# Performance work log

Hardware: AMD Instinct MI355X
Metric: run time of the kernel (lower is better)

The kernel has to match this reference:

```python
import jax, jax.numpy as jnp
import numpy as np

ALPHA = 0.1       # args.alpha
T = 1.0           # args.T temperature
SIGMA = 64.0      # Gaussian kernel bandwidth of kernel_function
B_CONST = 1.0     # B in get_lambda
N_ITERS = 50      # 2^-50 << tol=1e-8, matches the break condition of the 1000-iter loop
HW = 256          # image resolution (upsample target)


def _features(feat):
    # get_feature: bilinear upsample (align_corners=False == half-pixel, as jax.image.resize) then sigmoid(x/T)
    n, c, _, _ = feat.shape
    up = jax.image.resize(feat, (n, c, HW, HW), method='bilinear')
    return jax.nn.sigmoid(up / T)


def setup_inputs() -> dict:
    key = jax.random.key(0)
    k1, k2, k3, k4 = jax.random.split(key, 4)
    return {
        'cal_feat': jax.random.normal(k1, (256, 1, 64, 64), jnp.float32),
        'test_feat': jax.random.normal(k2, (32, 1, 64, 64), jnp.float32),
        'cal_gt': jax.random.randint(k3, (256, 1, 256, 256), 0, 2, jnp.int32),
        'test_gt': jax.random.randint(k4, (32, 1, 256, 256), 0, 2, jnp.int32),
    }


def reference(cal_feat, test_feat, cal_gt, test_gt):
    cal_res = _features(cal_feat)    # [N,1,H,W] in (0,1)
    test_res = _features(test_feat)  # [B,1,H,W]
    N = cal_res.shape[0]
    B = test_res.shape[0]
    f32 = cal_res.dtype

    # kernel_function.get_weight: Gaussian RBF on flattened features, plus self-weight 1, row-normalized -> [B, N+1]
    cf = cal_res.reshape(N, -1)
    tf = test_res.reshape(B, -1)
    d2 = (tf * tf).sum(-1)[:, None] + (cf * cf).sum(-1)[None, :] - 2.0 * (tf @ cf.T)
    k = jnp.exp(-d2 / (2.0 * SIGMA * SIGMA))
    w = jnp.concatenate([k, jnp.ones((B, 1), f32)], axis=1)
    w = w / w.sum(axis=1, keepdims=True)

    # FNR_i(t) = #{positive pixels of cal sample i with score < t} / #positives
    # (pred = res >= t, so false negatives are positive pixels with res < t). Precompute sorted
    # positive-pixel scores per cal sample so the bisection is a batched searchsorted.
    gt = (cal_gt > 0).reshape(N, -1)
    pos = jnp.sum(gt, axis=1)                                    # [N]
    scores = jnp.where(gt, cal_res.reshape(N, -1), jnp.inf)
    sorted_scores = jnp.sort(scores, axis=1)                     # [N, HW*HW], padding at +inf
    pos_f = jnp.maximum(pos, 1).astype(f32)

    def fnr_at(t):  # t: [B] thresholds -> [N, B]
        cnt = jax.vmap(lambda s: jnp.searchsorted(s, t, side='left'))(sorted_scores)
        return cnt.astype(f32) / pos_f[:, None]

    # batched bisection on lambda (get_lambda, vectorized over the B test samples)
    def body(carry, _):
        low, high = carry
        lam = 0.5 * (low + high)
        fnr = fnr_at(1.0 - lam)                                   # [N, B]
        risk = jnp.einsum('bn,nb->b', w[:, :-1], fnr) + w[:, -1] * B_CONST
        high = jnp.where(risk < ALPHA, lam, high)
        low = jnp.where(risk >= ALPHA, lam, low)
        return (low, high), None

    init = (jnp.zeros((B,), f32), jnp.ones((B,), f32))
    (low, _), _ = jax.lax.scan(body, init, None, length=N_ITERS)
    lam = low  # _lambda = low after the loop

    # prediction set, size and per-test FNR (get_fnr_list on the test sample)
    pred = test_res >= (1.0 - lam)[:, None, None, None]           # [B,1,H,W] bool
    size = jnp.sum(pred, axis=(1, 2, 3)).astype(f32)
    tgt = test_gt > 0
    tp = jnp.sum(pred & tgt, axis=(1, 2, 3)).astype(f32)
    tpos = jnp.maximum(jnp.sum(tgt, axis=(1, 2, 3)), 1).astype(f32)
    fnr_test = 1.0 - tp / tpos                                    # fdr_tensor, [B]
    return fnr_test, lam, size
```

## Files before the change

kernel.cpp:

```cpp
#include <hip/hip_runtime.h>


#define NPIX 65536
#define HB 16256
#define CDF_STRIDE 16272
#define ALPHA 0.1f
#define STAGE_CAP 40960

#define OFF_TESTRES  0
#define OFF_CALBF    8388608u
#define OFF_TESTBF   41943040u
#define OFF_GROUPED  46137344u
#define OFF_CDF      79691776u
#define OFF_GPART    96354304u
#define OFF_CC       98451456u
#define OFF_TT       98452480u
#define OFF_THR      98452608u
#define OFF_LAM      98452736u
#define OFF_FACC     98452864u

typedef __attribute__((ext_vector_type(8))) short bf16x8;
typedef __attribute__((ext_vector_type(16))) float f32x16;

__device__ __forceinline__ unsigned short f2bf_rne(float f) {
  unsigned u = __float_as_uint(f);
  return (unsigned short)((u + 0x7FFFu + ((u >> 16) & 1u)) >> 16);
}

__device__ __forceinline__ int SW(int w) { return w ^ ((w >> 5) & 31); }

__device__ __forceinline__ float score_at(const float* __restrict__ sfeat,
                                          int x0, int x1, float wx, int y) {
  float sy = 0.25f * (float)y - 0.375f;
  int y0 = (int)floorf(sy);
  float wy = sy - (float)y0;
  int y1 = y0 + 1;
  if (y0 < 0) y0 = 0;
  if (y1 > 63) y1 = 63;
  float a = sfeat[y0 * 64 + x0] * (1.f - wx) + sfeat[y0 * 64 + x1] * wx;
  float b = sfeat[y1 * 64 + x0] * (1.f - wx) + sfeat[y1 * 64 + x1] * wx;
  float v = a * (1.f - wy) + b * wy;
  return 1.f / (1.f + __expf(-v));
}

__global__ __launch_bounds__(1024, 2) void k_calt(const float* __restrict__ featc,
                                                  const int* __restrict__ gt,
                                                  unsigned short* __restrict__ calbf,
                                                  unsigned* __restrict__ cdf,
                                                  unsigned short* __restrict__ grouped,
                                                  float* __restrict__ cc,
                                                  const float* __restrict__ featt,
                                                  float* __restrict__ tres,
                                                  unsigned short* __restrict__ tbf) {
  __shared__ unsigned smem[9264];
  __shared__ float sfeat[4096];
  __shared__ float tfeat[4096];
  __shared__ unsigned short sstage[STAGE_CAP];
  const int tid = threadIdx.x;
  const int lane = tid & 63, wv = tid >> 6;
  const int x = tid & 255, yq = tid >> 8;
  float sx = 0.25f * (float)x - 0.375f;
  int x0 = (int)floorf(sx);
  float wx = sx - (float)x0;
  int x1 = x0 + 1;
  if (x0 < 0) x0 = 0;
  if (x1 > 63) x1 = 63;

  const int n = blockIdx.x;
  const int b = n >> 3, sl = n & 7;
  for (int i = tid; i < 8192; i += 1024) smem[i] = 0;
  for (int i = tid; i < 4096; i += 1024) {
    sfeat[i] = featc[n * 4096 + i];
    tfeat[i] = featt[b * 4096 + i];
  }
  const int* gtn = gt + (size_t)n * NPIX;
  unsigned short* cbn = calbf + (size_t)n * NPIX;
  __syncthreads();

  {
    float* resb = tres + (size_t)b * NPIX + sl * 8192;
    unsigned short* tbn = tbf + (size_t)b * NPIX + sl * 8192;
    #pragma unroll
    for (int i = 0; i < 8; ++i) {
      int y = sl * 32 + i * 4 + yq;
      float s = score_at(tfeat, x0, x1, wx, y);
      int q = i * 1024 + tid;
      resb[q] = s;
      tbn[q] = f2bf_rne(s);
    }
  }

  unsigned long long pm = 0ull;
  float sumsq = 0.f;
  #pragma unroll 8
  for (int it = 0; it < 64; ++it) {
    int y = it * 4 + yq;
    float s = score_at(sfeat, x0, x1, wx, y);
    int p = (y << 8) + x;
    unsigned short bh = f2bf_rne(s);
    cbn[p] = bh;
    float sr = __uint_as_float((unsigned)bh << 16);
    sumsq += sr * sr;
    if (gtn[p] > 0) {
      pm |= (1ull << it);
      unsigned bits = __float_as_uint(s);
      atomicAdd(&smem[SW((int)(bits >> 17))], (bits & 0x10000u) ? 0x10000u : 1u);
    }
  }
  #pragma unroll
  for (int off = 32; off; off >>= 1) sumsq += __shfl_xor(sumsq, off);
  if (lane == 0) smem[8208 + wv] = __float_as_uint(sumsq);
  __syncthreads();
  if (tid == 0) {
    float c = 0.f;
    for (int w = 0; w < 16; ++w) c += __uint_as_float(smem[8208 + w]);
    cc[n] = c;
  }
  const int wbase = tid * 8;
  unsigned psum = 0;
  #pragma unroll
  for (int j = 0; j < 8; ++j) {
    unsigned w = smem[SW(wbase + j)];
    psum += (w & 0xFFFFu) + (w >> 16);
  }
  unsigned inc = psum;
  #pragma unroll
  for (int off = 1; off < 64; off <<= 1) {
    unsigned v = __shfl_up(inc, off);
    if (lane >= off) inc += v;
  }
  if (lane == 63) smem[8192 + wv] = inc;
  smem[8224 + tid] = inc - psum;
  __syncthreads();
  {
    unsigned woff = 0;
    for (int w = 0; w < wv; ++w) woff += smem[8192 + w];
    unsigned run = woff + smem[8224 + tid];
    #pragma unroll
    for (int j = 0; j < 8; ++j) {
      int si = SW(wbase + j);
      unsigned w = smem[si];
      unsigned clo = run;
      run += (w & 0xFFFFu);
      unsigned chi = run;
      run += (w >> 16);
      smem[si] = (chi << 16) | clo;
    }
    if (tid == 1023) smem[9248] = run;
  }
  __syncthreads();
  unsigned* cdfn = cdf + (size_t)n * CDF_STRIDE;
  for (int i = tid; i < HB; i += 1024) {
    unsigned w = smem[SW(i >> 1)];
    cdfn[i] = (i & 1) ? (w >> 16) : (w & 0xFFFFu);
  }
  const unsigned pos = smem[9248];
  if (tid == 0) cdfn[HB] = pos;
  __syncthreads();
  unsigned short* gn = grouped + (size_t)n * NPIX;
  for (int it = 0; it < 64; ++it) {
    if (pm & (1ull << it)) {
      int y = it * 4 + yq;
      float s = score_at(sfeat, x0, x1, wx, y);
      unsigned bits = __float_as_uint(s);
      unsigned old = atomicAdd(&smem[SW((int)(bits >> 17))], (bits & 0x10000u) ? 0x10000u : 1u);
      unsigned idx = (bits & 0x10000u) ? (old >> 16) : (old & 0xFFFFu);
      unsigned short lo = (unsigned short)(bits & 0xFFFFu);
      if (idx < STAGE_CAP) sstage[idx] = lo;
      else gn[idx] = lo;
    }
  }
  __syncthreads();
  unsigned lim = pos < STAGE_CAP ? pos : STAGE_CAP;
  for (unsigned i = tid; i < lim; i += 1024) gn[i] = sstage[i];
}

__global__ __launch_bounds__(1024) void k_tt(const unsigned short* __restrict__ tbf,
                                             float* __restrict__ tt) {
  __shared__ unsigned smem[16];
  const int tid = threadIdx.x;
  const int lane = tid & 63, wv = tid >> 6;
  const int x = tid & 255, yq = tid >> 8;
  const int b = blockIdx.x;
  const unsigned short* tbn = tbf + (size_t)b * NPIX;
  float sumsq = 0.f;
  #pragma unroll 4
  for (int it = 0; it < 64; ++it) {
    int p = ((it * 4 + yq) << 8) + x;
    float sr = __uint_as_float((unsigned)tbn[p] << 16);
    sumsq += sr * sr;
  }
  #pragma unroll
  for (int off = 32; off; off >>= 1) sumsq += __shfl_xor(sumsq, off);
  if (lane == 0) smem[wv] = __float_as_uint(sumsq);
  __syncthreads();
  if (tid == 0) {
    float t = 0.f;
    for (int w = 0; w < 16; ++w) t += __uint_as_float(smem[w]);
    tt[b] = t;
  }
}

__global__ __launch_bounds__(256) void k_gemm(const unsigned short* __restrict__ tbf,
                                              const unsigned short* __restrict__ cbf,
                                              float* __restrict__ gpart) {
  __shared__ __align__(16) unsigned short As[16384];
  __shared__ __align__(16) unsigned short Bs[16384];
  __shared__ float lred[4][1024];
  const int tid = threadIdx.x;
  const int lane = tid & 63, wv = tid >> 6;
  const int r = lane & 31, half = lane >> 5;
  const int nt = blockIdx.x;
  f32x16 acc;
  #pragma unroll
  for (int i = 0; i < 16; ++i) acc[i] = 0.f;
  for (int ch = 0; ch < 2; ++ch) {
    const size_t kbase = (size_t)blockIdx.y * 1024 + ch * 512;
    __syncthreads();
    #pragma unroll
    for (int s = 0; s < 16; ++s) {
      int flat = s * 256 + tid;
      int rem = flat & 2047;
      int row = rem >> 6, kb = rem & 63;
      const unsigned short* src = (flat >= 2048)
          ? cbf + (size_t)(nt * 32 + row) * NPIX + kbase + kb * 8
          : tbf + (size_t)row * NPIX + kbase + kb * 8;
      int slot = ((kb << 5) + row) ^ (kb & 31);
      int4 v = *(const int4*)src;
      *(int4*)((flat >= 2048 ? Bs : As) + slot * 8) = v;
    }
    __syncthreads();
    #pragma unroll
    for (int i = 0; i < 8; ++i) {
      int k8 = (wv << 4) + i * 2 + half;
      int slot = ((k8 << 5) + r) ^ (k8 & 31);
      bf16x8 a = *(const bf16x8*)(As + slot * 8);
      bf16x8 b = *(const bf16x8*)(Bs + slot * 8);
      acc = __builtin_amdgcn_mfma_f32_32x32x16_bf16(a, b, acc, 0, 0, 0);
    }
  }
  #pragma unroll
  for (int rg = 0; rg < 16; ++rg) {
    int m = (rg & 3) + 8 * (rg >> 2) + 4 * half;
    lred[wv][m * 32 + r] = acc[rg];
  }
  __syncthreads();
  float* gp = gpart + (size_t)(blockIdx.y * 8 + nt) * 1024;
  for (int e = tid; e < 1024; e += 256)
    gp[e] = lred[0][e] + lred[1][e] + lred[2][e] + lred[3][e];
}

__global__ __launch_bounds__(512) void k_quant(const float* __restrict__ gpart,
                                               const float* __restrict__ cc,
                                               const float* __restrict__ tt,
                                               const unsigned* __restrict__ cdf,
                                               const unsigned short* __restrict__ grouped,
                                               float* __restrict__ lam,
                                               float* __restrict__ thr,
                                               int* __restrict__ facc) {
  __shared__ float qs[256];
  __shared__ float bins[4096];
  __shared__ float red[8];
  __shared__ float bc[2];
  __shared__ unsigned sBin;
  const int b = blockIdx.x, tid = threadIdx.x;
  const int lane = tid & 63, wv = tid >> 6;

  if (tid < 4) facc[b * 4 + tid] = 0;
  for (int i = tid; i < 4096; i += 512) bins[i] = 0.f;
  if (tid == 0) sBin = 0xFFFFFFFFu;

  float k = 0.f;
  if (tid < 256) {
    const float* gp = gpart + ((tid >> 5) * 1024) + (b * 32) + (tid & 31);
    float g = 0.f;
    #pragma unroll 8
    for (int ks = 0; ks < 64; ++ks) g += gp[(size_t)ks * 8192];
    float d2 = tt[b] + cc[tid] - 2.f * g;
    k = expf(-d2 * (1.f / 8192.f));
  }
  float v = k;
  #pragma unroll
  for (int off = 32; off; off >>= 1) v += __shfl_xor(v, off);
  if (lane == 0) red[wv] = v;
  __syncthreads();
  if (tid == 0) {
    float ws = 1.f;
    for (int w = 0; w < 8; ++w) ws += red[w];
    bc[0] = ws;
  }
  __syncthreads();
  const float wsum = bc[0];
  const float wlast = 1.f / wsum;
  const float R = ALPHA - wlast;
  if (R <= 0.f) {
    if (tid == 0) { lam[b] = 1.0f; thr[b] = 0.0f; }
    return;
  }
  if (tid < 256) {
    unsigned pos = cdf[(size_t)tid * CDF_STRIDE + HB];
    qs[tid] = k / (wsum * (float)(pos ? pos : 1u));
  }
  __syncthreads();

  int lo = 0, hi = HB;
  float baseS = 0.f;
  for (int it = 0; it < 14; ++it) {
    int mid = (lo + hi) >> 1;
    float p = 0.f;
    if (tid < 256) p = qs[tid] * (float)cdf[(size_t)tid * CDF_STRIDE + mid];
    float r = p;
    #pragma unroll
    for (int off = 32; off; off >>= 1) r += __shfl_xor(r, off);
    if (lane == 0) red[wv] = r;
    __syncthreads();
    if (tid == 0) {
      float s = 0.f;
      for (int w = 0; w < 8; ++w) s += red[w];
      bc[1] = s;
    }
    __syncthreads();
    float S = bc[1];
    if (S < R) { lo = mid; baseS = S; } else { hi = mid; }
  }
  const int B = lo;

  {
    const int n = tid >> 1;
    const float q = qs[n];
    const unsigned* cn = cdf + (size_t)n * CDF_STRIDE;
    const unsigned short* gn = grouped + (size_t)n * NPIX;
    unsigned e0 = cn[B + 1];
    for (unsigned j = cn[B] + (tid & 1); j < e0; j += 2)
      atomicAdd(&bins[gn[j] >> 4], q);
  }
  __syncthreads();

  if (wv == 0) {
    float s = 0.f;
    for (int j = 0; j < 64; ++j) s += bins[lane * 64 + j];
    float inc = s;
    #pragma unroll
    for (int off = 1; off < 64; off <<= 1) {
      float u = __shfl_up(inc, off);
      if (lane >= off) inc += u;
    }
    float pre = inc - s;
    bool hit = (baseS + pre < R) && (baseS + inc >= R);
    unsigned long long m = __ballot(hit);
    int ow = m ? (__ffsll((unsigned long long)m) - 1) : -1;
    if (lane == ow) {
      float run = baseS + pre;
      unsigned bin = (unsigned)lane * 64 + 63;
      for (int j = 0; j < 64; ++j) {
        float bv = bins[lane * 64 + j];
        if (run + bv >= R) { bin = (unsigned)lane * 64 + j; break; }
        run += bv;
      }
      sBin = bin;
    }
    if (m == 0 && lane == 0) sBin = 4095u;
  }
  __syncthreads();
  if (tid == 0) {
    unsigned tb = ((unsigned)B << 16) | (sBin << 4);
    lam[b] = 1.0f - __uint_as_float(tb | 0x8u);
    thr[b] = __uint_as_float((tb | 0xFu) + 1u);
  }
}

__global__ __launch_bounds__(256) void k_finalp(const float* __restrict__ tres,
                                                const int* __restrict__ tgt,
                                                const float* __restrict__ thr,
                                                int* __restrict__ facc) {
  __shared__ int red[12];
  const int b = blockIdx.x, seg = blockIdx.y, tid = threadIdx.x;
  const int lane = tid & 63, wv = tid >> 6;
  const float th = thr[b];
  const float4* rb4 = (const float4*)(tres + (size_t)b * NPIX + seg * 8192);
  const int4* gb4 = (const int4*)(tgt + (size_t)b * NPIX + seg * 8192);
  int sz = 0, tp = 0, tpos = 0;
  #pragma unroll
  for (int i = 0; i < 8; ++i) {
    float4 r4 = rb4[i * 256 + tid];
    int4 g4 = gb4[i * 256 + tid];
    int p0 = (r4.x >= th), t0 = (g4.x > 0);
    int p1 = (r4.y >= th), t1 = (g4.y > 0);
    int p2 = (r4.z >= th), t2 = (g4.z > 0);
    int p3 = (r4.w >= th), t3 = (g4.w > 0);
    sz += p0 + p1 + p2 + p3;
    tp += (p0 & t0) + (p1 & t1) + (p2 & t2) + (p3 & t3);
    tpos += t0 + t1 + t2 + t3;
  }
  #pragma unroll
  for (int off = 32; off; off >>= 1) {
    sz += __shfl_xor(sz, off);
    tp += __shfl_xor(tp, off);
    tpos += __shfl_xor(tpos, off);
  }
  if (lane == 0) { red[wv] = sz; red[4 + wv] = tp; red[8 + wv] = tpos; }
  __syncthreads();
  if (tid == 0) {
    int s0 = red[0] + red[1] + red[2] + red[3];
    int s1 = red[4] + red[5] + red[6] + red[7];
    int s2 = red[8] + red[9] + red[10] + red[11];
    atomicAdd(&facc[b * 4 + 0], s0);
    atomicAdd(&facc[b * 4 + 1], s1);
    atomicAdd(&facc[b * 4 + 2], s2);
  }
}

__global__ void k_out(const int* __restrict__ facc, const float* __restrict__ lam,
                      float* __restrict__ out) {
  int b = threadIdx.x;
  if (b < 32) {
    int sz = facc[b * 4], tp = facc[b * 4 + 1], tpos = facc[b * 4 + 2];
    float tposf = (float)(tpos > 0 ? tpos : 1);
    out[b] = 1.f - (float)tp / tposf;
    out[32 + b] = lam[b];
    out[64 + b] = (float)sz;
  }
}

extern "C" void kernel_launch(void* const* d_in, const int* in_sizes, int n_in,
                              void* d_out, int out_size, void* d_ws, size_t ws_size,
                              hipStream_t stream) {
  const float* cal_feat = (const float*)d_in[0];
  const float* test_feat = (const float*)d_in[1];
  const int* cal_gt = (const int*)d_in[2];
  const int* test_gt = (const int*)d_in[3];
  float* out = (float*)d_out;
  char* ws = (char*)d_ws;

  float* test_res = (float*)(ws + OFF_TESTRES);
  unsigned short* cal_bf = (unsigned short*)(ws + OFF_CALBF);
  unsigned short* test_bf = (unsigned short*)(ws + OFF_TESTBF);
  unsigned short* grouped = (unsigned short*)(ws + OFF_GROUPED);
  unsigned* cdf = (unsigned*)(ws + OFF_CDF);
  float* gpart = (float*)(ws + OFF_GPART);
  float* cc = (float*)(ws + OFF_CC);
  float* tt = (float*)(ws + OFF_TT);
  float* thr = (float*)(ws + OFF_THR);
  float* lam = (float*)(ws + OFF_LAM);
  int* facc = (int*)(ws + OFF_FACC);

  k_calt<<<dim3(256), dim3(1024), 0, stream>>>(cal_feat, cal_gt, cal_bf, cdf, grouped, cc,
                                               test_feat, test_res, test_bf);
  k_tt<<<dim3(32), dim3(1024), 0, stream>>>(test_bf, tt);
  k_gemm<<<dim3(8, 64), dim3(256), 0, stream>>>(test_bf, cal_bf, gpart);
  k_quant<<<dim3(32), dim3(512), 0, stream>>>(gpart, cc, tt, cdf, grouped, lam, thr, facc);
  k_finalp<<<dim3(32, 8), dim3(256), 0, stream>>>(test_res, test_gt, thr, facc);
  k_out<<<dim3(1), dim3(64), 0, stream>>>(facc, lam, out);
}
```

Baseline: 246.9 us.

## Fuse test norm, quantile search, final stats and output into one kernel

Folds the test squared-norm reduction, threshold search, per-test FNR/size accumulation and output writing into a single kernel, removing three launches and the global atomics and intermediate buffers between them. Separately, the upsample in k_calt now reuses each horizontally interpolated row across consecutive output rows in a rolling fashion instead of recomputing both source rows per pixel. The final pass now runs over 32 blocks instead of 256, so the 8 MB test score/gt scan gets less parallelism and may take longer than the separate kernel did.

```diff
diff --git a/kernel.cpp b/kernel.cpp
--- a/kernel.cpp
+++ b/kernel.cpp
@@ -14,10 +14,6 @@
 #define OFF_CDF      79691776u
 #define OFF_GPART    96354304u
 #define OFF_CC       98451456u
-#define OFF_TT       98452480u
-#define OFF_THR      98452608u
-#define OFF_LAM      98452736u
-#define OFF_FACC     98452864u
 
 typedef __attribute__((ext_vector_type(8))) short bf16x8;
 typedef __attribute__((ext_vector_type(16))) float f32x16;
@@ -29,6 +25,14 @@
 
 __device__ __forceinline__ int SW(int w) { return w ^ ((w >> 5) & 31); }
 
+__device__ __forceinline__ float hrow_at(const float* __restrict__ f, int x0, int x1,
+                                         float wx, int r) {
+  return f[r * 64 + x0] * (1.f - wx) + f[r * 64 + x1] * wx;
+}
+__device__ __forceinline__ float sig_v(float a, float b, float wy) {
+  float v = a * (1.f - wy) + b * wy;
+  return 1.f / (1.f + __expf(-v));
+}
 __device__ __forceinline__ float score_at(const float* __restrict__ sfeat,
                                           int x0, int x1, float wx, int y) {
   float sy = 0.25f * (float)y - 0.375f;
@@ -37,10 +41,9 @@
   int y1 = y0 + 1;
   if (y0 < 0) y0 = 0;
   if (y1 > 63) y1 = 63;
-  float a = sfeat[y0 * 64 + x0] * (1.f - wx) + sfeat[y0 * 64 + x1] * wx;
-  float b = sfeat[y1 * 64 + x0] * (1.f - wx) + sfeat[y1 * 64 + x1] * wx;
-  float v = a * (1.f - wy) + b * wy;
-  return 1.f / (1.f + __expf(-v));
+  float a = hrow_at(sfeat, x0, x1, wx, y0);
+  float b = hrow_at(sfeat, x0, x1, wx, y1);
+  return sig_v(a, b, wy);
 }
 
 __global__ __launch_bounds__(1024, 2) void k_calt(const float* __restrict__ featc,
@@ -65,6 +68,9 @@
   int x1 = x0 + 1;
   if (x0 < 0) x0 = 0;
   if (x1 > 63) x1 = 63;
+  const float syq = 0.25f * (float)yq - 0.375f;
+  const int c0 = (int)floorf(syq);
+  const float wy = syq - (float)c0;
 
   const int n = blockIdx.x;
   const int b = n >> 3, sl = n & 7;
@@ -80,10 +86,16 @@
   {
     float* resb = tres + (size_t)b * NPIX + sl * 8192;
     unsigned short* tbn = tbf + (size_t)b * NPIX + sl * 8192;
+    int r0 = sl * 8 + c0;
+    if (r0 < 0) r0 = 0;
+    float hprev = hrow_at(tfeat, x0, x1, wx, r0);
     #pragma unroll
     for (int i = 0; i < 8; ++i) {
-      int y = sl * 32 + i * 4 + yq;
-      float s = score_at(tfeat, x0, x1, wx, y);
+      int r1 = sl * 8 + i + c0 + 1;
+      if (r1 > 63) r1 = 63;
+      float hb = hrow_at(tfeat, x0, x1, wx, r1);
+      float s = sig_v(hprev, hb, wy);
+      hprev = hb;
       int q = i * 1024 + tid;
       resb[q] = s;
       tbn[q] = f2bf_rne(s);
@@ -92,19 +104,26 @@
 
   unsigned long long pm = 0ull;
   float sumsq = 0.f;
-  #pragma unroll 8
-  for (int it = 0; it < 64; ++it) {
-    int y = it * 4 + yq;
-    float s = score_at(sfeat, x0, x1, wx, y);
-    int p = (y << 8) + x;
-    unsigned short bh = f2bf_rne(s);
-    cbn[p] = bh;
-    float sr = __uint_as_float((unsigned)bh << 16);
-    sumsq += sr * sr;
-    if (gtn[p] > 0) {
-      pm |= (1ull << it);
-      unsigned bits = __float_as_uint(s);
-      atomicAdd(&smem[SW((int)(bits >> 17))], (bits & 0x10000u) ? 0x10000u : 1u);
+  {
+    int r0 = c0 < 0 ? 0 : c0;
+    float hprev = hrow_at(sfeat, x0, x1, wx, r0);
+    #pragma unroll 8
+    for (int it = 0; it < 64; ++it) {
+      int r1 = it + c0 + 1;
+      if (r1 > 63) r1 = 63;
+      float hb = hrow_at(sfeat, x0, x1, wx, r1);
+      float s = sig_v(hprev, hb, wy);
+      hprev = hb;
+      int p = ((it * 4 + yq) << 8) + x;
+      unsigned short bh = f2bf_rne(s);
+      cbn[p] = bh;
+      float sr = __uint_as_float((unsigned)bh << 16);
+      sumsq += sr * sr;
+      if (gtn[p] > 0) {
+        pm |= (1ull << it);
+        unsigned bits = __float_as_uint(s);
+        atomicAdd(&smem[SW((int)(bits >> 17))], (bits & 0x10000u) ? 0x10000u : 1u);
+      }
     }
   }
   #pragma unroll
@@ -173,32 +192,6 @@
   __syncthreads();
   unsigned lim = pos < STAGE_CAP ? pos : STAGE_CAP;
   for (unsigned i = tid; i < lim; i += 1024) gn[i] = sstage[i];
-}
-
-__global__ __launch_bounds__(1024) void k_tt(const unsigned short* __restrict__ tbf,
-                                             float* __restrict__ tt) {
-  __shared__ unsigned smem[16];
-  const int tid = threadIdx.x;
-  const int lane = tid & 63, wv = tid >> 6;
-  const int x = tid & 255, yq = tid >> 8;
-  const int b = blockIdx.x;
-  const unsigned short* tbn = tbf + (size_t)b * NPIX;
-  float sumsq = 0.f;
-  #pragma unroll 4
-  for (int it = 0; it < 64; ++it) {
-    int p = ((it * 4 + yq) << 8) + x;
-    float sr = __uint_as_float((unsigned)tbn[p] << 16);
-    sumsq += sr * sr;
-  }
-  #pragma unroll
-  for (int off = 32; off; off >>= 1) sumsq += __shfl_xor(sumsq, off);
-  if (lane == 0) smem[wv] = __float_as_uint(sumsq);
-  __syncthreads();
-  if (tid == 0) {
-    float t = 0.f;
-    for (int w = 0; w < 16; ++w) t += __uint_as_float(smem[w]);
-    tt[b] = t;
-  }
 }
 
 __global__ __launch_bounds__(256) void k_gemm(const unsigned short* __restrict__ tbf,
@@ -250,33 +243,62 @@
     gp[e] = lred[0][e] + lred[1][e] + lred[2][e] + lred[3][e];
 }
 
-__global__ __launch_bounds__(512) void k_quant(const float* __restrict__ gpart,
-                                               const float* __restrict__ cc,
-                                               const float* __restrict__ tt,
-                                               const unsigned* __restrict__ cdf,
-                                               const unsigned short* __restrict__ grouped,
-                                               float* __restrict__ lam,
-                                               float* __restrict__ thr,
-                                               int* __restrict__ facc) {
+__global__ __launch_bounds__(512) void k_quantf(const float* __restrict__ gpart,
+                                                const float* __restrict__ cc,
+                                                const unsigned short* __restrict__ tbf,
+                                                const unsigned* __restrict__ cdf,
+                                                const unsigned short* __restrict__ grouped,
+                                                const float* __restrict__ tres,
+                                                const int* __restrict__ tgt,
+                                                float* __restrict__ out) {
   __shared__ float qs[256];
   __shared__ float bins[4096];
   __shared__ float red[8];
-  __shared__ float bc[2];
+  __shared__ float tpart[16];
+  __shared__ float bc[6];
+  __shared__ int ired[24];
   __shared__ unsigned sBin;
   const int b = blockIdx.x, tid = threadIdx.x;
   const int lane = tid & 63, wv = tid >> 6;
 
-  if (tid < 4) facc[b * 4 + tid] = 0;
   for (int i = tid; i < 4096; i += 512) bins[i] = 0.f;
   if (tid == 0) sBin = 0xFFFFFFFFu;
 
+  {
+    const unsigned short* tbn = tbf + (size_t)b * NPIX;
+    const int xa = tid & 255, ya = tid >> 8;
+    const int yb = ya + 2;
+    float sa = 0.f, sb = 0.f;
+    #pragma unroll 4
+    for (int it = 0; it < 64; ++it) {
+      float ra = __uint_as_float((unsigned)tbn[((it * 4 + ya) << 8) + xa] << 16);
+      float rb = __uint_as_float((unsigned)tbn[((it * 4 + yb) << 8) + xa] << 16);
+      sa += ra * ra;
+      sb += rb * rb;
+    }
+    #pragma unroll
+    for (int off = 32; off; off >>= 1) {
+      sa += __shfl_xor(sa, off);
+      sb += __shfl_xor(sb, off);
+    }
+    if (lane == 0) { tpart[wv] = sa; tpart[8 + wv] = sb; }
+  }
+  __syncthreads();
+  if (tid == 0) {
+    float t = 0.f;
+    for (int w = 0; w < 16; ++w) t += tpart[w];
+    bc[2] = t;
+  }
+  float g = 0.f;
+  if (tid < 256) {
+    const float* gp = gpart + ((tid >> 5) * 1024) + (b * 32) + (tid & 31);
+    #pragma unroll 8
+    for (int ks = 0; ks < 64; ++ks) g += gp[(size_t)ks * 8192];
+  }
+  __syncthreads();
   float k = 0.f;
   if (tid < 256) {
-    const float* gp = gpart + ((tid >> 5) * 1024) + (b * 32) + (tid & 31);
-    float g = 0.f;
-    #pragma unroll 8
-    for (int ks = 0; ks < 64; ++ks) g += gp[(size_t)ks * 8192];
-    float d2 = tt[b] + cc[tid] - 2.f * g;
+    float d2 = bc[2] + cc[tid] - 2.f * g;
     k = expf(-d2 * (1.f / 8192.f));
   }
   float v = k;
@@ -293,97 +315,89 @@
   const float wsum = bc[0];
   const float wlast = 1.f / wsum;
   const float R = ALPHA - wlast;
-  if (R <= 0.f) {
-    if (tid == 0) { lam[b] = 1.0f; thr[b] = 0.0f; }
-    return;
-  }
-  if (tid < 256) {
-    unsigned pos = cdf[(size_t)tid * CDF_STRIDE + HB];
-    qs[tid] = k / (wsum * (float)(pos ? pos : 1u));
-  }
-  __syncthreads();
-
-  int lo = 0, hi = HB;
-  float baseS = 0.f;
-  for (int it = 0; it < 14; ++it) {
-    int mid = (lo + hi) >> 1;
-    float p = 0.f;
-    if (tid < 256) p = qs[tid] * (float)cdf[(size_t)tid * CDF_STRIDE + mid];
-    float r = p;
-    #pragma unroll
-    for (int off = 32; off; off >>= 1) r += __shfl_xor(r, off);
-    if (lane == 0) red[wv] = r;
+
+  if (R > 0.f) {
+    if (tid < 256) {
+      unsigned pos = cdf[(size_t)tid * CDF_STRIDE + HB];
+      qs[tid] = k / (wsum * (float)(pos ? pos : 1u));
+    }
+    __syncthreads();
+    int lo = 0, hi = HB;
+    float baseS = 0.f;
+    for (int it = 0; it < 14; ++it) {
+      int mid = (lo + hi) >> 1;
+      float p = 0.f;
+      if (tid < 256) p = qs[tid] * (float)cdf[(size_t)tid * CDF_STRIDE + mid];
+      float r = p;
+      #pragma unroll
+      for (int off = 32; off; off >>= 1) r += __shfl_xor(r, off);
+      if (lane == 0) red[wv] = r;
+      __syncthreads();
+      if (tid == 0) {
+        float s = 0.f;
+        for (int w = 0; w < 8; ++w) s += red[w];
+        bc[1] = s;
+      }
+      __syncthreads();
+      float S = bc[1];
+      if (S < R) { lo = mid; baseS = S; } else { hi = mid; }
+    }
+    const int B = lo;
+
+    {
+      const int n = tid >> 1;
+      const float q = qs[n];
+      const unsigned* cn = cdf + (size_t)n * CDF_STRIDE;
+      const unsigned short* gn = grouped + (size_t)n * NPIX;
+      unsigned e0 = cn[B + 1];
+      for (unsigned j = cn[B] + (tid & 1); j < e0; j += 2)
+        atomicAdd(&bins[gn[j] >> 4], q);
+    }
+    __syncthreads();
+
+    if (wv == 0) {
+      float s = 0.f;
+      for (int j = 0; j < 64; ++j) s += bins[lane * 64 + j];
+      float inc = s;
+      #pragma unroll
+      for (int off = 1; off < 64; off <<= 1) {
+        float u = __shfl_up(inc, off);
+        if (lane >= off) inc += u;
+      }
+      float pre = inc - s;
+      bool hit = (baseS + pre < R) && (baseS + inc >= R);
+      unsigned long long m = __ballot(hit);
+      int ow = m ? (__ffsll((unsigned long long)m) - 1) : -1;
+      if (lane == ow) {
+        float run = baseS + pre;
+        unsigned bin = (unsigned)lane * 64 + 63;
+        for (int j = 0; j < 64; ++j) {
+          float bv = bins[lane * 64 + j];
+          if (run + bv >= R) { bin = (unsigned)lane * 64 + j; break; }
+          run += bv;
+        }
+        sBin = bin;
+      }
+      if (m == 0 && lane == 0) sBin = 4095u;
+    }
     __syncthreads();
     if (tid == 0) {
-      float s = 0.f;
-      for (int w = 0; w < 8; ++w) s += red[w];
-      bc[1] = s;
-    }
-    __syncthreads();
-    float S = bc[1];
-    if (S < R) { lo = mid; baseS = S; } else { hi = mid; }
-  }
-  const int B = lo;
-
-  {
-    const int n = tid >> 1;
-    const float q = qs[n];
-    const unsigned* cn = cdf + (size_t)n * CDF_STRIDE;
-    const unsigned short* gn = grouped + (size_t)n * NPIX;
-    unsigned e0 = cn[B + 1];
-    for (unsigned j = cn[B] + (tid & 1); j < e0; j += 2)
-      atomicAdd(&bins[gn[j] >> 4], q);
-  }
-  __syncthreads();
-
-  if (wv == 0) {
-    float s = 0.f;
-    for (int j = 0; j < 64; ++j) s += bins[lane * 64 + j];
-    float inc = s;
-    #pragma unroll
-    for (int off = 1; off < 64; off <<= 1) {
-      float u = __shfl_up(inc, off);
-      if (lane >= off) inc += u;
-    }
-    float pre = inc - s;
-    bool hit = (baseS + pre < R) && (baseS + inc >= R);
-    unsigned long long m = __ballot(hit);
-    int ow = m ? (__ffsll((unsigned long long)m) - 1) : -1;
-    if (lane == ow) {
-      float run = baseS + pre;
-      unsigned bin = (unsigned)lane * 64 + 63;
-      for (int j = 0; j < 64; ++j) {
-        float bv = bins[lane * 64 + j];
-        if (run + bv >= R) { bin = (unsigned)lane * 64 + j; break; }
-        run += bv;
-      }
-      sBin = bin;
-    }
-    if (m == 0 && lane == 0) sBin = 4095u;
-  }
-  __syncthreads();
-  if (tid == 0) {
-    unsigned tb = ((unsigned)B << 16) | (sBin << 4);
-    lam[b] = 1.0f - __uint_as_float(tb | 0x8u);
-    thr[b] = __uint_as_float((tb | 0xFu) + 1u);
-  }
-}
-
-__global__ __launch_bounds__(256) void k_finalp(const float* __restrict__ tres,
-                                                const int* __restrict__ tgt,
-                                                const float* __restrict__ thr,
-                                                int* __restrict__ facc) {
-  __shared__ int red[12];
-  const int b = blockIdx.x, seg = blockIdx.y, tid = threadIdx.x;
-  const int lane = tid & 63, wv = tid >> 6;
-  const float th = thr[b];
-  const float4* rb4 = (const float4*)(tres + (size_t)b * NPIX + seg * 8192);
-  const int4* gb4 = (const int4*)(tgt + (size_t)b * NPIX + seg * 8192);
+      unsigned tb = ((unsigned)B << 16) | (sBin << 4);
+      bc[5] = 1.0f - __uint_as_float(tb | 0x8u);
+      bc[3] = __uint_as_float((tb | 0xFu) + 1u);
+    }
+  } else {
+    if (tid == 0) { bc[5] = 1.0f; bc[3] = 0.0f; }
+  }
+  __syncthreads();
+
+  const float th = bc[3];
+  const float4* rb4 = (const float4*)(tres + (size_t)b * NPIX);
+  const int4* gb4 = (const int4*)(tgt + (size_t)b * NPIX);
   int sz = 0, tp = 0, tpos = 0;
-  #pragma unroll
-  for (int i = 0; i < 8; ++i) {
-    float4 r4 = rb4[i * 256 + tid];
-    int4 g4 = gb4[i * 256 + tid];
+  for (int i = tid; i < 16384; i += 512) {
+    float4 r4 = rb4[i];
+    int4 g4 = gb4[i];
     int p0 = (r4.x >= th), t0 = (g4.x > 0);
     int p1 = (r4.y >= th), t1 = (g4.y > 0);
     int p2 = (r4.z >= th), t2 = (g4.z > 0);
@@ -398,27 +412,15 @@
     tp += __shfl_xor(tp, off);
     tpos += __shfl_xor(tpos, off);
   }
-  if (lane == 0) { red[wv] = sz; red[4 + wv] = tp; red[8 + wv] = tpos; }
+  if (lane == 0) { ired[wv] = sz; ired[8 + wv] = tp; ired[16 + wv] = tpos; }
   __syncthreads();
   if (tid == 0) {
-    int s0 = red[0] + red[1] + red[2] + red[3];
-    int s1 = red[4] + red[5] + red[6] + red[7];
-    int s2 = red[8] + red[9] + red[10] + red[11];
-    atomicAdd(&facc[b * 4 + 0], s0);
-    atomicAdd(&facc[b * 4 + 1], s1);
-    atomicAdd(&facc[b * 4 + 2], s2);
-  }
-}
-
-__global__ void k_out(const int* __restrict__ facc, const float* __restrict__ lam,
-                      float* __restrict__ out) {
-  int b = threadIdx.x;
-  if (b < 32) {
-    int sz = facc[b * 4], tp = facc[b * 4 + 1], tpos = facc[b * 4 + 2];
-    float tposf = (float)(tpos > 0 ? tpos : 1);
-    out[b] = 1.f - (float)tp / tposf;
-    out[32 + b] = lam[b];
-    out[64 + b] = (float)sz;
+    int s0 = 0, s1 = 0, s2 = 0;
+    for (int w = 0; w < 8; ++w) { s0 += ired[w]; s1 += ired[8 + w]; s2 += ired[16 + w]; }
+    float tposf = (float)(s2 > 0 ? s2 : 1);
+    out[b] = 1.f - (float)s1 / tposf;
+    out[32 + b] = bc[5];
+    out[64 + b] = (float)s0;
   }
 }
 
@@ -439,16 +441,10 @@
   unsigned* cdf = (unsigned*)(ws + OFF_CDF);
   float* gpart = (float*)(ws + OFF_GPART);
   float* cc = (float*)(ws + OFF_CC);
-  float* tt = (float*)(ws + OFF_TT);
-  float* thr = (float*)(ws + OFF_THR);
-  float* lam = (float*)(ws + OFF_LAM);
-  int* facc = (int*)(ws + OFF_FACC);
 
   k_calt<<<dim3(256), dim3(1024), 0, stream>>>(cal_feat, cal_gt, cal_bf, cdf, grouped, cc,
                                                test_feat, test_res, test_bf);
-  k_tt<<<dim3(32), dim3(1024), 0, stream>>>(test_bf, tt);
   k_gemm<<<dim3(8, 64), dim3(256), 0, stream>>>(test_bf, cal_bf, gpart);
-  k_quant<<<dim3(32), dim3(512), 0, stream>>>(gpart, cc, tt, cdf, grouped, lam, thr, facc);
-  k_finalp<<<dim3(32, 8), dim3(256), 0, stream>>>(test_res, test_gt, thr, facc);
-  k_out<<<dim3(1), dim3(64), 0, stream>>>(facc, lam, out);
-}
+  k_quantf<<<dim3(32), dim3(512), 0, stream>>>(gpart, cc, test_bf, cdf, grouped,
+                                               test_res, test_gt, out);
+}
```

Result: slower. 254.2 us (+3.0%).

## Fold test sum-of-squares into quantile kernel and widen histogram counters to 32 bits

Applied to the files above, without the earlier changes.

Removes the separate k_tt launch: the test-row squared-norm reduction now runs inside the quantile kernel (renamed k_quantw) on 512 threads, and its loads of gpart are overlapped with that reduction. In the calibration kernel the 16-bit packed histogram counters become full 32-bit bins. This removes the pack/unpack logic in both the scan and the scatter passes. The extra shared memory is paid for by aliasing the test-feature buffer onto the staging buffer and shrinking the staging capacity, so more of the scatter may fall back to global writes. The goal is to cut one launch and some ALU work in the scan/scatter.

```diff
diff --git a/kernel.cpp b/kernel.cpp
--- a/kernel.cpp
+++ b/kernel.cpp
@@ -5,7 +5,7 @@
 #define HB 16256
 #define CDF_STRIDE 16272
 #define ALPHA 0.1f
-#define STAGE_CAP 40960
+#define STAGE_CAP 35840
 
 #define OFF_TESTRES  0
 #define OFF_CALBF    8388608u
@@ -14,10 +14,9 @@
 #define OFF_CDF      79691776u
 #define OFF_GPART    96354304u
 #define OFF_CC       98451456u
-#define OFF_TT       98452480u
-#define OFF_THR      98452608u
-#define OFF_LAM      98452736u
-#define OFF_FACC     98452864u
+#define OFF_THR      98452480u
+#define OFF_LAM      98452608u
+#define OFF_FACC     98452736u
 
 typedef __attribute__((ext_vector_type(8))) short bf16x8;
 typedef __attribute__((ext_vector_type(16))) float f32x16;
@@ -52,10 +51,10 @@
                                                   const float* __restrict__ featt,
                                                   float* __restrict__ tres,
                                                   unsigned short* __restrict__ tbf) {
-  __shared__ unsigned smem[9264];
+  __shared__ unsigned smem[17313];
   __shared__ float sfeat[4096];
-  __shared__ float tfeat[4096];
-  __shared__ unsigned short sstage[STAGE_CAP];
+  __shared__ __align__(16) unsigned short sstage[STAGE_CAP];
+  float* tfeat = (float*)sstage;
   const int tid = threadIdx.x;
   const int lane = tid & 63, wv = tid >> 6;
   const int x = tid & 255, yq = tid >> 8;
@@ -68,7 +67,7 @@
 
   const int n = blockIdx.x;
   const int b = n >> 3, sl = n & 7;
-  for (int i = tid; i < 8192; i += 1024) smem[i] = 0;
+  for (int i = tid; i < HB; i += 1024) smem[i] = 0;
   for (int i = tid; i < 4096; i += 1024) {
     sfeat[i] = featc[n * 4096 + i];
     tfeat[i] = featt[b * 4096 + i];
@@ -103,25 +102,23 @@
     sumsq += sr * sr;
     if (gtn[p] > 0) {
       pm |= (1ull << it);
-      unsigned bits = __float_as_uint(s);
-      atomicAdd(&smem[SW((int)(bits >> 17))], (bits & 0x10000u) ? 0x10000u : 1u);
+      atomicAdd(&smem[SW((int)(__float_as_uint(s) >> 16))], 1u);
     }
   }
   #pragma unroll
   for (int off = 32; off; off >>= 1) sumsq += __shfl_xor(sumsq, off);
-  if (lane == 0) smem[8208 + wv] = __float_as_uint(sumsq);
+  if (lane == 0) smem[16272 + wv] = __float_as_uint(sumsq);
   __syncthreads();
   if (tid == 0) {
     float c = 0.f;
-    for (int w = 0; w < 16; ++w) c += __uint_as_float(smem[8208 + w]);
+    for (int w = 0; w < 16; ++w) c += __uint_as_float(smem[16272 + w]);
     cc[n] = c;
   }
-  const int wbase = tid * 8;
+  const int base = tid * 16;
   unsigned psum = 0;
-  #pragma unroll
-  for (int j = 0; j < 8; ++j) {
-    unsigned w = smem[SW(wbase + j)];
-    psum += (w & 0xFFFFu) + (w >> 16);
+  if (tid < 1016) {
+    #pragma unroll
+    for (int j = 0; j < 16; ++j) psum += smem[SW(base + j)];
   }
   unsigned inc = psum;
   #pragma unroll
@@ -129,32 +126,28 @@
     unsigned v = __shfl_up(inc, off);
     if (lane >= off) inc += v;
   }
-  if (lane == 63) smem[8192 + wv] = inc;
-  smem[8224 + tid] = inc - psum;
+  if (lane == 63) smem[16256 + wv] = inc;
+  smem[16288 + tid] = inc - psum;
   __syncthreads();
   {
     unsigned woff = 0;
-    for (int w = 0; w < wv; ++w) woff += smem[8192 + w];
-    unsigned run = woff + smem[8224 + tid];
-    #pragma unroll
-    for (int j = 0; j < 8; ++j) {
-      int si = SW(wbase + j);
-      unsigned w = smem[si];
-      unsigned clo = run;
-      run += (w & 0xFFFFu);
-      unsigned chi = run;
-      run += (w >> 16);
-      smem[si] = (chi << 16) | clo;
-    }
-    if (tid == 1023) smem[9248] = run;
+    for (int w = 0; w < wv; ++w) woff += smem[16256 + w];
+    unsigned run = woff + smem[16288 + tid];
+    if (tid < 1016) {
+      #pragma unroll
+      for (int j = 0; j < 16; ++j) {
+        int si = SW(base + j);
+        unsigned h = smem[si];
+        smem[si] = run;
+        run += h;
+      }
+    }
+    if (tid == 1015) smem[17312] = run;
   }
   __syncthreads();
   unsigned* cdfn = cdf + (size_t)n * CDF_STRIDE;
-  for (int i = tid; i < HB; i += 1024) {
-    unsigned w = smem[SW(i >> 1)];
-    cdfn[i] = (i & 1) ? (w >> 16) : (w & 0xFFFFu);
-  }
-  const unsigned pos = smem[9248];
+  for (int i = tid; i < HB; i += 1024) cdfn[i] = smem[SW(i)];
+  const unsigned pos = smem[17312];
   if (tid == 0) cdfn[HB] = pos;
   __syncthreads();
   unsigned short* gn = grouped + (size_t)n * NPIX;
@@ -163,8 +156,7 @@
       int y = it * 4 + yq;
       float s = score_at(sfeat, x0, x1, wx, y);
       unsigned bits = __float_as_uint(s);
-      unsigned old = atomicAdd(&smem[SW((int)(bits >> 17))], (bits & 0x10000u) ? 0x10000u : 1u);
-      unsigned idx = (bits & 0x10000u) ? (old >> 16) : (old & 0xFFFFu);
+      unsigned idx = atomicAdd(&smem[SW((int)(bits >> 16))], 1u);
       unsigned short lo = (unsigned short)(bits & 0xFFFFu);
       if (idx < STAGE_CAP) sstage[idx] = lo;
       else gn[idx] = lo;
@@ -173,32 +165,6 @@
   __syncthreads();
   unsigned lim = pos < STAGE_CAP ? pos : STAGE_CAP;
   for (unsigned i = tid; i < lim; i += 1024) gn[i] = sstage[i];
-}
-
-__global__ __launch_bounds__(1024) void k_tt(const unsigned short* __restrict__ tbf,
-                                             float* __restrict__ tt) {
-  __shared__ unsigned smem[16];
-  const int tid = threadIdx.x;
-  const int lane = tid & 63, wv = tid >> 6;
-  const int x = tid & 255, yq = tid >> 8;
-  const int b = blockIdx.x;
-  const unsigned short* tbn = tbf + (size_t)b * NPIX;
-  float sumsq = 0.f;
-  #pragma unroll 4
-  for (int it = 0; it < 64; ++it) {
-    int p = ((it * 4 + yq) << 8) + x;
-    float sr = __uint_as_float((unsigned)tbn[p] << 16);
-    sumsq += sr * sr;
-  }
-  #pragma unroll
-  for (int off = 32; off; off >>= 1) sumsq += __shfl_xor(sumsq, off);
-  if (lane == 0) smem[wv] = __float_as_uint(sumsq);
-  __syncthreads();
-  if (tid == 0) {
-    float t = 0.f;
-    for (int w = 0; w < 16; ++w) t += __uint_as_float(smem[w]);
-    tt[b] = t;
-  }
 }
 
 __global__ __launch_bounds__(256) void k_gemm(const unsigned short* __restrict__ tbf,
@@ -250,18 +216,19 @@
     gp[e] = lred[0][e] + lred[1][e] + lred[2][e] + lred[3][e];
 }
 
-__global__ __launch_bounds__(512) void k_quant(const float* __restrict__ gpart,
-                                               const float* __restrict__ cc,
-                                               const float* __restrict__ tt,
-                                               const unsigned* __restrict__ cdf,
-                                               const unsigned short* __restrict__ grouped,
-                                               float* __restrict__ lam,
-                                               float* __restrict__ thr,
-                                               int* __restrict__ facc) {
+__global__ __launch_bounds__(512) void k_quantw(const float* __restrict__ gpart,
+                                                const float* __restrict__ cc,
+                                                const unsigned short* __restrict__ tbf,
+                                                const unsigned* __restrict__ cdf,
+                                                const unsigned short* __restrict__ grouped,
+                                                float* __restrict__ lam,
+                                                float* __restrict__ thr,
+                                                int* __restrict__ facc) {
   __shared__ float qs[256];
   __shared__ float bins[4096];
   __shared__ float red[8];
-  __shared__ float bc[2];
+  __shared__ float tpart[16];
+  __shared__ float bc[3];
   __shared__ unsigned sBin;
   const int b = blockIdx.x, tid = threadIdx.x;
   const int lane = tid & 63, wv = tid >> 6;
@@ -270,13 +237,41 @@
   for (int i = tid; i < 4096; i += 512) bins[i] = 0.f;
   if (tid == 0) sBin = 0xFFFFFFFFu;
 
+  {
+    const unsigned short* tbn = tbf + (size_t)b * NPIX;
+    const int xa = tid & 255, ya = tid >> 8;
+    const int yb = ya + 2;
+    float sa = 0.f, sb = 0.f;
+    #pragma unroll 4
+    for (int it = 0; it < 64; ++it) {
+      float ra = __uint_as_float((unsigned)tbn[((it * 4 + ya) << 8) + xa] << 16);
+      float rb = __uint_as_float((unsigned)tbn[((it * 4 + yb) << 8) + xa] << 16);
+      sa += ra * ra;
+      sb += rb * rb;
+    }
+    #pragma unroll
+    for (int off = 32; off; off >>= 1) {
+      sa += __shfl_xor(sa, off);
+      sb += __shfl_xor(sb, off);
+    }
+    if (lane == 0) { tpart[wv] = sa; tpart[8 + wv] = sb; }
+  }
+  __syncthreads();
+  if (tid == 0) {
+    float t = 0.f;
+    for (int w = 0; w < 16; ++w) t += tpart[w];
+    bc[2] = t;
+  }
+  float g = 0.f;
+  if (tid < 256) {
+    const float* gp = gpart + ((tid >> 5) * 1024) + (b * 32) + (tid & 31);
+    #pragma unroll 8
+    for (int ks = 0; ks < 64; ++ks) g += gp[(size_t)ks * 8192];
+  }
+  __syncthreads();
   float k = 0.f;
   if (tid < 256) {
-    const float* gp = gpart + ((tid >> 5) * 1024) + (b * 32) + (tid & 31);
-    float g = 0.f;
-    #pragma unroll 8
-    for (int ks = 0; ks < 64; ++ks) g += gp[(size_t)ks * 8192];
-    float d2 = tt[b] + cc[tid] - 2.f * g;
+    float d2 = bc[2] + cc[tid] - 2.f * g;
     k = expf(-d2 * (1.f / 8192.f));
   }
   float v = k;
@@ -439,16 +434,15 @@
   unsigned* cdf = (unsigned*)(ws + OFF_CDF);
   float* gpart = (float*)(ws + OFF_GPART);
   float* cc = (float*)(ws + OFF_CC);
-  float* tt = (float*)(ws + OFF_TT);
   float* thr = (float*)(ws + OFF_THR);
   float* lam = (float*)(ws + OFF_LAM);
   int* facc = (int*)(ws + OFF_FACC);
 
   k_calt<<<dim3(256), dim3(1024), 0, stream>>>(cal_feat, cal_gt, cal_bf, cdf, grouped, cc,
                                                test_feat, test_res, test_bf);
-  k_tt<<<dim3(32), dim3(1024), 0, stream>>>(test_bf, tt);
   k_gemm<<<dim3(8, 64), dim3(256), 0, stream>>>(test_bf, cal_bf, gpart);
-  k_quant<<<dim3(32), dim3(512), 0, stream>>>(gpart, cc, tt, cdf, grouped, lam, thr, facc);
+  k_quantw<<<dim3(32), dim3(512), 0, stream>>>(gpart, cc, test_bf, cdf, grouped,
+                                               lam, thr, facc);
   k_finalp<<<dim3(32, 8), dim3(256), 0, stream>>>(test_res, test_gt, thr, facc);
   k_out<<<dim3(1), dim3(64), 0, stream>>>(facc, lam, out);
 }
```

Result: no change. 242.7 us (-1.7%).
